# Optimization experiments

Measured on AMD Instinct MI355X. Metric: run time of the kernel, lower is better.

## Reference

```python
import jax, jax.numpy as jnp
import numpy as np

U, I, D, E = 8192, 8192, 64, 1048576  # users, items, emb dim, nnz of adjacency


def spmm(row, col, val, x, n):
    """Sparse (COO) @ dense: y[r] += val * x[c], like torch.sparse.mm."""
    return jax.ops.segment_sum(val[:, None] * x[col], row, num_segments=n)


def setup_inputs() -> dict:
    key = jax.random.key(0)
    k1, k2, k3, k4, k5, k6 = jax.random.split(key, 6)
    users_emb = jax.random.normal(k1, (U, D), dtype=jnp.float32) * 0.1  # nn.init.normal_(std=0.1)
    items_emb = jax.random.normal(k2, (I, D), dtype=jnp.float32) * 0.1
    edge_row = jax.random.randint(k3, (E,), 0, U + I, dtype=jnp.int32)
    edge_col = jax.random.randint(k4, (E,), 0, U + I, dtype=jnp.int32)
    # positive normalized adjacency values (stand-in for D^-1/2 A D^-1/2 entries)
    edge_val = jax.random.uniform(k5, (E,), dtype=jnp.float32) / 64.0
    # sparse 0/1 interaction matrix densified, as in labels = interaction_mat.toarray()
    labels = (jax.random.uniform(k6, (U, I)) < 0.02).astype(jnp.float32)
    return {"users_emb": users_emb, "items_emb": items_emb,
            "edge_row": edge_row, "edge_col": edge_col,
            "edge_val": edge_val, "labels": labels, "n_layers": 3}


def reference(users_emb, items_emb, edge_row, edge_col, edge_val, labels, n_layers):
    n = users_emb.shape[0] + items_emb.shape[0]
    u = users_emb.shape[0]
    all_emb = jnp.concatenate([users_emb, items_emb], axis=0)  # [n, D]
    # stack + mean over (n_layers+1) layer outputs == online accumulation
    acc = all_emb
    for _ in range(n_layers):
        all_emb = spmm(edge_row, edge_col, edge_val, all_emb, n)
        acc = acc + all_emb
    light_out = acc / jnp.float32(n_layers + 1)
    user_emb = light_out[:u]   # [U, D]
    item_emb = light_out[u:]   # [I, D]
    scores = user_emb @ item_emb.T  # [U, I]
    # BCEWithLogitsLoss (mean reduction): logaddexp(0, s) - s*y
    loss = jnp.mean(jnp.logaddexp(jnp.float32(0.0), scores) - scores * labels)
    return (loss, user_emb, item_emb)
```

## Files before the change

### kernel.cpp

```cpp
#include <hip/hip_runtime.h>

#define U_N 8192
#define I_N 8192
#define N_N 16384
#define D_N 64
#define E_N 1048576
#define CAP 128

typedef __attribute__((ext_vector_type(8)))  short short8;
typedef __attribute__((ext_vector_type(16))) float f32x16;


__global__ void k_prep(const float* __restrict__ ue, const float* __restrict__ ie,
                       float* __restrict__ cur, float* __restrict__ acc,
                       unsigned* __restrict__ cnt, float* __restrict__ lossp) {
    int i = blockIdx.x * blockDim.x + threadIdx.x;
    const int HU = U_N * D_N / 4;
    float4 v = (i < HU) ? ((const float4*)ue)[i] : ((const float4*)ie)[i - HU];
    ((float4*)cur)[i] = v;
    ((float4*)acc)[i] = v;
    if (i < N_N / 4) ((uint4*)cnt)[i] = make_uint4(0, 0, 0, 0);
    if (i == 0) *lossp = 0.f;
}

__global__ void k_bucket(const int* __restrict__ row, const int* __restrict__ col,
                         const float* __restrict__ val, unsigned* __restrict__ cnt,
                         int2* __restrict__ buckets) {
    int e = blockIdx.x * blockDim.x + threadIdx.x;
    if (e < E_N) {
        int r = row[e];
        unsigned p = atomicAdd(&cnt[r], 1u);
        if (p < CAP) buckets[(size_t)r * CAP + p] = make_int2(col[e], __float_as_int(val[e]));
    }
}

__global__ void k_spmm(const unsigned* __restrict__ cnt, const int4* __restrict__ bk4,
                       const float* __restrict__ x, float* __restrict__ y,
                       float* __restrict__ acc) {
    int wave = (int)((blockIdx.x * blockDim.x + threadIdx.x) >> 6);
    int lane = threadIdx.x & 63;
    if (wave >= N_N) return;
    int n = (int)cnt[wave]; n = n > CAP ? CAP : n;
    const int4* bp = bk4 + (size_t)wave * (CAP / 2);
    float a = 0.f;
    int j = 0;
    for (; j + 8 <= n; j += 8) {
        int4 q0 = bp[j / 2 + 0], q1 = bp[j / 2 + 1];
        int4 q2 = bp[j / 2 + 2], q3 = bp[j / 2 + 3];
        float x0 = x[q0.x * 64 + lane], x1 = x[q0.z * 64 + lane];
        float x2 = x[q1.x * 64 + lane], x3 = x[q1.z * 64 + lane];
        float x4 = x[q2.x * 64 + lane], x5 = x[q2.z * 64 + lane];
        float x6 = x[q3.x * 64 + lane], x7 = x[q3.z * 64 + lane];
        a = fmaf(__int_as_float(q0.y), x0, a); a = fmaf(__int_as_float(q0.w), x1, a);
        a = fmaf(__int_as_float(q1.y), x2, a); a = fmaf(__int_as_float(q1.w), x3, a);
        a = fmaf(__int_as_float(q2.y), x4, a); a = fmaf(__int_as_float(q2.w), x5, a);
        a = fmaf(__int_as_float(q3.y), x6, a); a = fmaf(__int_as_float(q3.w), x7, a);
    }
    const int2* bp2 = (const int2*)bp;
    for (; j < n; ++j) {
        int2 q = bp2[j];
        a = fmaf(__int_as_float(q.y), x[q.x * 64 + lane], a);
    }
    y[wave * 64 + lane] = a;
    acc[wave * 64 + lane] += a;
}

__global__ void k_spmm_last(const unsigned* __restrict__ cnt, const int4* __restrict__ bk4,
                            const float* __restrict__ x, const float* __restrict__ acc,
                            float* __restrict__ o, ushort* __restrict__ bfemb) {
    int wave = (int)((blockIdx.x * blockDim.x + threadIdx.x) >> 6);
    int lane = threadIdx.x & 63;
    if (wave >= N_N) return;
    int n = (int)cnt[wave]; n = n > CAP ? CAP : n;
    const int4* bp = bk4 + (size_t)wave * (CAP / 2);
    float a = 0.f;
    int j = 0;
    for (; j + 8 <= n; j += 8) {
        int4 q0 = bp[j / 2 + 0], q1 = bp[j / 2 + 1];
        int4 q2 = bp[j / 2 + 2], q3 = bp[j / 2 + 3];
        float x0 = x[q0.x * 64 + lane], x1 = x[q0.z * 64 + lane];
        float x2 = x[q1.x * 64 + lane], x3 = x[q1.z * 64 + lane];
        float x4 = x[q2.x * 64 + lane], x5 = x[q2.z * 64 + lane];
        float x6 = x[q3.x * 64 + lane], x7 = x[q3.z * 64 + lane];
        a = fmaf(__int_as_float(q0.y), x0, a); a = fmaf(__int_as_float(q0.w), x1, a);
        a = fmaf(__int_as_float(q1.y), x2, a); a = fmaf(__int_as_float(q1.w), x3, a);
        a = fmaf(__int_as_float(q2.y), x4, a); a = fmaf(__int_as_float(q2.w), x5, a);
        a = fmaf(__int_as_float(q3.y), x6, a); a = fmaf(__int_as_float(q3.w), x7, a);
    }
    const int2* bp2 = (const int2*)bp;
    for (; j < n; ++j) {
        int2 q = bp2[j];
        a = fmaf(__int_as_float(q.y), x[q.x * 64 + lane], a);
    }
    int idx = wave * 64 + lane;
    float l = (acc[idx] + a) * 0.25f;
    o[idx] = l;
    union { float f; unsigned u; } c; c.f = l;
    bfemb[idx] = (ushort)((c.u + 0x7fffu + ((c.u >> 16) & 1u)) >> 16);
}

__global__ __launch_bounds__(256) void k_gemm_loss(const ushort* __restrict__ bfemb,
                                                   const float* __restrict__ labels,
                                                   float* __restrict__ lossp) {
    __shared__ float red[4];
    int tid  = threadIdx.x;
    int lane = tid & 63;
    int w    = tid >> 6;
    int wr   = w >> 1, wc = w & 1;
    int row0 = blockIdx.y * 128 + wr * 64;
    int col0 = blockIdx.x * 128 + wc * 64;

    int lrow = lane & 31;
    int lk   = (lane >> 5) * 8;

    short8 a[2][4], b[2][4];
    #pragma unroll
    for (int fi = 0; fi < 2; ++fi) {
        const ushort* pa = bfemb + (size_t)(row0 + fi * 32 + lrow) * 64 + lk;
        const ushort* pb = bfemb + (size_t)(U_N + col0 + fi * 32 + lrow) * 64 + lk;
        #pragma unroll
        for (int kk = 0; kk < 4; ++kk) {
            a[fi][kk] = *(const short8*)(pa + kk * 16);
            b[fi][kk] = *(const short8*)(pb + kk * 16);
        }
    }

    f32x16 acc00 = {}, acc01 = {}, acc10 = {}, acc11 = {};
    #pragma unroll
    for (int kk = 0; kk < 4; ++kk) {
        acc00 = __builtin_amdgcn_mfma_f32_32x32x16_bf16(a[0][kk], b[0][kk], acc00, 0, 0, 0);
        acc01 = __builtin_amdgcn_mfma_f32_32x32x16_bf16(a[0][kk], b[1][kk], acc01, 0, 0, 0);
        acc10 = __builtin_amdgcn_mfma_f32_32x32x16_bf16(a[1][kk], b[0][kk], acc10, 0, 0, 0);
        acc11 = __builtin_amdgcn_mfma_f32_32x32x16_bf16(a[1][kk], b[1][kk], acc11, 0, 0, 0);
    }

    const float LN2 = 0.69314718055994531f;
    const float C2  = 0.125f;
    const float C4  = -1.0f / 192.0f;

    float sum = 0.f, maxa = 0.f;
    int rsub = (lane >> 5) * 4;
    #pragma unroll
    for (int fi = 0; fi < 2; ++fi) {
        #pragma unroll
        for (int fj = 0; fj < 2; ++fj) {
            const f32x16& ac = fi ? (fj ? acc11 : acc10) : (fj ? acc01 : acc00);
            int gcol = col0 + fj * 32 + (lane & 31);
            #pragma unroll
            for (int q = 0; q < 4; ++q) {
                #pragma unroll
                for (int r = 0; r < 4; ++r) {
                    int grow = row0 + fi * 32 + q * 8 + rsub + r;
                    float s = ac[q * 4 + r];
                    float lab = labels[(size_t)grow * 8192 + gcol];
                    float s2 = s * s;
                    float t = fmaf(s2, fmaf(s2, C4, C2), fmaf(s, 0.5f, LN2));
                    sum += t;
                    sum = fmaf(-s, lab, sum);
                    maxa = fmaxf(maxa, fabsf(s));
                }
            }
        }
    }

    if (__any(maxa > 1.0f)) {
        sum = 0.f;
        #pragma unroll
        for (int fi = 0; fi < 2; ++fi) {
            #pragma unroll
            for (int fj = 0; fj < 2; ++fj) {
                const f32x16& ac = fi ? (fj ? acc11 : acc10) : (fj ? acc01 : acc00);
                int gcol = col0 + fj * 32 + (lane & 31);
                #pragma unroll
                for (int q = 0; q < 4; ++q) {
                    #pragma unroll
                    for (int r = 0; r < 4; ++r) {
                        int grow = row0 + fi * 32 + q * 8 + rsub + r;
                        float s = ac[q * 4 + r];
                        float lab = labels[(size_t)grow * 8192 + gcol];
                        float t = fmaxf(s, 0.f) + __logf(1.f + __expf(-fabsf(s)));
                        sum += t - s * lab;
                    }
                }
            }
        }
    }

    #pragma unroll
    for (int off = 32; off > 0; off >>= 1) sum += __shfl_down(sum, off);
    if ((tid & 63) == 0) red[w] = sum;
    __syncthreads();
    if (tid == 0) atomicAdd(lossp, red[0] + red[1] + red[2] + red[3]);
}

__global__ void k_finish(const float* __restrict__ lossp, float* __restrict__ out) {
    out[0] = *lossp * (1.0f / 67108864.0f);
}

extern "C" void kernel_launch(void* const* d_in, const int* in_sizes, int n_in,
                              void* d_out, int out_size, void* d_ws, size_t ws_size,
                              hipStream_t stream) {
    const float* ue     = (const float*)d_in[0];
    const float* ie     = (const float*)d_in[1];
    const int*   erow   = (const int*)d_in[2];
    const int*   ecol   = (const int*)d_in[3];
    const float* eval_  = (const float*)d_in[4];
    const float* labels = (const float*)d_in[5];
    float* out = (float*)d_out;

    char* ws = (char*)d_ws;
    unsigned* cnt     = (unsigned*)(ws + 0);
    float*    lossp   = (float*)   (ws + 65536);
    int2*     buckets = (int2*)    (ws + 1048576);
    float*    emb0    = (float*)   (ws + 18874368);
    float*    emb1    = (float*)   (ws + 23068672);
    float*    accb    = (float*)   (ws + 27262976);
    ushort*   bfemb   = (ushort*)emb1;

    k_prep<<<1024, 256, 0, stream>>>(ue, ie, emb0, accb, cnt, lossp);
    k_bucket<<<4096, 256, 0, stream>>>(erow, ecol, eval_, cnt, buckets);

    const int4* bk4 = (const int4*)buckets;
    k_spmm<<<4096, 256, 0, stream>>>(cnt, bk4, emb0, emb1, accb);
    k_spmm<<<4096, 256, 0, stream>>>(cnt, bk4, emb1, emb0, accb);
    k_spmm_last<<<4096, 256, 0, stream>>>(cnt, bk4, emb0, accb, out + 1, bfemb);

    dim3 g(64, 64);
    k_gemm_loss<<<g, 256, 0, stream>>>(bfemb, labels, lossp);
    k_finish<<<1, 1, 0, stream>>>(lossp, out);
}
```

Before: 245.3 us.

## Store layer embeddings in bf16, pad bucket counters, fold finish into loss kernel

The intermediate layer embeddings read by the SpMM gathers are now stored as bf16, which halves gather traffic, while the layer accumulator stays in fp32. Bucket counters are spaced 16 words apart to reduce atomic contention from sharing the same cache line. The loss epilogue accumulates power sums of the scores and applies the series once per lane, and the separate finish kernel is replaced by a last-block-done counter. Rounding each layer's input to bf16 adds precision loss that compounds across layers.

```diff
diff --git a/kernel.cpp b/kernel.cpp
--- a/kernel.cpp
+++ b/kernel.cpp
@@ -1,26 +1,36 @@
 #include <hip/hip_runtime.h>
 
 #define U_N 8192
-#define I_N 8192
 #define N_N 16384
-#define D_N 64
 #define E_N 1048576
 #define CAP 128
+#define CSTRIDE 16
 
 typedef __attribute__((ext_vector_type(8)))  short short8;
 typedef __attribute__((ext_vector_type(16))) float f32x16;
 
 
+__device__ __forceinline__ float bfu(ushort u) {
+    union { unsigned v; float f; } c; c.v = (unsigned)u << 16; return c.f;
+}
+__device__ __forceinline__ ushort f2bf(float f) {
+    union { float f; unsigned u; } c; c.f = f;
+    return (ushort)((c.u + 0x7fffu + ((c.u >> 16) & 1u)) >> 16);
+}
+
 __global__ void k_prep(const float* __restrict__ ue, const float* __restrict__ ie,
-                       float* __restrict__ cur, float* __restrict__ acc,
-                       unsigned* __restrict__ cnt, float* __restrict__ lossp) {
+                       ushort* __restrict__ xb, float* __restrict__ acc,
+                       unsigned* __restrict__ cnt, float* __restrict__ lossp,
+                       unsigned* __restrict__ done) {
     int i = blockIdx.x * blockDim.x + threadIdx.x;
-    const int HU = U_N * D_N / 4;
+    const int HU = U_N * 64 / 4;
     float4 v = (i < HU) ? ((const float4*)ue)[i] : ((const float4*)ie)[i - HU];
-    ((float4*)cur)[i] = v;
     ((float4*)acc)[i] = v;
-    if (i < N_N / 4) ((uint4*)cnt)[i] = make_uint4(0, 0, 0, 0);
-    if (i == 0) *lossp = 0.f;
+    ushort4 b;
+    b.x = f2bf(v.x); b.y = f2bf(v.y); b.z = f2bf(v.z); b.w = f2bf(v.w);
+    ((ushort4*)xb)[i] = b;
+    if (i < 65536) ((uint4*)cnt)[i] = make_uint4(0, 0, 0, 0);
+    if (i == 0) { *lossp = 0.f; *done = 0u; }
 }
 
 __global__ void k_bucket(const int* __restrict__ row, const int* __restrict__ col,
@@ -29,28 +39,28 @@
     int e = blockIdx.x * blockDim.x + threadIdx.x;
     if (e < E_N) {
         int r = row[e];
-        unsigned p = atomicAdd(&cnt[r], 1u);
+        unsigned p = atomicAdd(&cnt[r * CSTRIDE], 1u);
         if (p < CAP) buckets[(size_t)r * CAP + p] = make_int2(col[e], __float_as_int(val[e]));
     }
 }
 
 __global__ void k_spmm(const unsigned* __restrict__ cnt, const int4* __restrict__ bk4,
-                       const float* __restrict__ x, float* __restrict__ y,
+                       const ushort* __restrict__ x, ushort* __restrict__ xo,
                        float* __restrict__ acc) {
     int wave = (int)((blockIdx.x * blockDim.x + threadIdx.x) >> 6);
     int lane = threadIdx.x & 63;
     if (wave >= N_N) return;
-    int n = (int)cnt[wave]; n = n > CAP ? CAP : n;
+    int n = (int)cnt[wave * CSTRIDE]; n = n > CAP ? CAP : n;
     const int4* bp = bk4 + (size_t)wave * (CAP / 2);
     float a = 0.f;
     int j = 0;
     for (; j + 8 <= n; j += 8) {
         int4 q0 = bp[j / 2 + 0], q1 = bp[j / 2 + 1];
         int4 q2 = bp[j / 2 + 2], q3 = bp[j / 2 + 3];
-        float x0 = x[q0.x * 64 + lane], x1 = x[q0.z * 64 + lane];
-        float x2 = x[q1.x * 64 + lane], x3 = x[q1.z * 64 + lane];
-        float x4 = x[q2.x * 64 + lane], x5 = x[q2.z * 64 + lane];
-        float x6 = x[q3.x * 64 + lane], x7 = x[q3.z * 64 + lane];
+        float x0 = bfu(x[q0.x * 64 + lane]), x1 = bfu(x[q0.z * 64 + lane]);
+        float x2 = bfu(x[q1.x * 64 + lane]), x3 = bfu(x[q1.z * 64 + lane]);
+        float x4 = bfu(x[q2.x * 64 + lane]), x5 = bfu(x[q2.z * 64 + lane]);
+        float x6 = bfu(x[q3.x * 64 + lane]), x7 = bfu(x[q3.z * 64 + lane]);
         a = fmaf(__int_as_float(q0.y), x0, a); a = fmaf(__int_as_float(q0.w), x1, a);
         a = fmaf(__int_as_float(q1.y), x2, a); a = fmaf(__int_as_float(q1.w), x3, a);
         a = fmaf(__int_as_float(q2.y), x4, a); a = fmaf(__int_as_float(q2.w), x5, a);
@@ -59,29 +69,30 @@
     const int2* bp2 = (const int2*)bp;
     for (; j < n; ++j) {
         int2 q = bp2[j];
-        a = fmaf(__int_as_float(q.y), x[q.x * 64 + lane], a);
-    }
-    y[wave * 64 + lane] = a;
-    acc[wave * 64 + lane] += a;
+        a = fmaf(__int_as_float(q.y), bfu(x[q.x * 64 + lane]), a);
+    }
+    int idx = wave * 64 + lane;
+    xo[idx] = f2bf(a);
+    acc[idx] += a;
 }
 
 __global__ void k_spmm_last(const unsigned* __restrict__ cnt, const int4* __restrict__ bk4,
-                            const float* __restrict__ x, const float* __restrict__ acc,
+                            const ushort* __restrict__ x, const float* __restrict__ acc,
                             float* __restrict__ o, ushort* __restrict__ bfemb) {
     int wave = (int)((blockIdx.x * blockDim.x + threadIdx.x) >> 6);
     int lane = threadIdx.x & 63;
     if (wave >= N_N) return;
-    int n = (int)cnt[wave]; n = n > CAP ? CAP : n;
+    int n = (int)cnt[wave * CSTRIDE]; n = n > CAP ? CAP : n;
     const int4* bp = bk4 + (size_t)wave * (CAP / 2);
     float a = 0.f;
     int j = 0;
     for (; j + 8 <= n; j += 8) {
         int4 q0 = bp[j / 2 + 0], q1 = bp[j / 2 + 1];
         int4 q2 = bp[j / 2 + 2], q3 = bp[j / 2 + 3];
-        float x0 = x[q0.x * 64 + lane], x1 = x[q0.z * 64 + lane];
-        float x2 = x[q1.x * 64 + lane], x3 = x[q1.z * 64 + lane];
-        float x4 = x[q2.x * 64 + lane], x5 = x[q2.z * 64 + lane];
-        float x6 = x[q3.x * 64 + lane], x7 = x[q3.z * 64 + lane];
+        float x0 = bfu(x[q0.x * 64 + lane]), x1 = bfu(x[q0.z * 64 + lane]);
+        float x2 = bfu(x[q1.x * 64 + lane]), x3 = bfu(x[q1.z * 64 + lane]);
+        float x4 = bfu(x[q2.x * 64 + lane]), x5 = bfu(x[q2.z * 64 + lane]);
+        float x6 = bfu(x[q3.x * 64 + lane]), x7 = bfu(x[q3.z * 64 + lane]);
         a = fmaf(__int_as_float(q0.y), x0, a); a = fmaf(__int_as_float(q0.w), x1, a);
         a = fmaf(__int_as_float(q1.y), x2, a); a = fmaf(__int_as_float(q1.w), x3, a);
         a = fmaf(__int_as_float(q2.y), x4, a); a = fmaf(__int_as_float(q2.w), x5, a);
@@ -90,18 +101,19 @@
     const int2* bp2 = (const int2*)bp;
     for (; j < n; ++j) {
         int2 q = bp2[j];
-        a = fmaf(__int_as_float(q.y), x[q.x * 64 + lane], a);
+        a = fmaf(__int_as_float(q.y), bfu(x[q.x * 64 + lane]), a);
     }
     int idx = wave * 64 + lane;
     float l = (acc[idx] + a) * 0.25f;
     o[idx] = l;
-    union { float f; unsigned u; } c; c.f = l;
-    bfemb[idx] = (ushort)((c.u + 0x7fffu + ((c.u >> 16) & 1u)) >> 16);
+    bfemb[idx] = f2bf(l);
 }
 
 __global__ __launch_bounds__(256) void k_gemm_loss(const ushort* __restrict__ bfemb,
                                                    const float* __restrict__ labels,
-                                                   float* __restrict__ lossp) {
+                                                   float* __restrict__ lossp,
+                                                   unsigned* __restrict__ done,
+                                                   float* __restrict__ out) {
     __shared__ float red[4];
     int tid  = threadIdx.x;
     int lane = tid & 63;
@@ -134,11 +146,7 @@
         acc11 = __builtin_amdgcn_mfma_f32_32x32x16_bf16(a[1][kk], b[1][kk], acc11, 0, 0, 0);
     }
 
-    const float LN2 = 0.69314718055994531f;
-    const float C2  = 0.125f;
-    const float C4  = -1.0f / 192.0f;
-
-    float sum = 0.f, maxa = 0.f;
+    float sum1 = 0.f, sum2 = 0.f, sum4 = 0.f, sumL = 0.f, m2 = 0.f;
     int rsub = (lane >> 5) * 4;
     #pragma unroll
     for (int fi = 0; fi < 2; ++fi) {
@@ -154,47 +162,50 @@
                     float s = ac[q * 4 + r];
                     float lab = labels[(size_t)grow * 8192 + gcol];
                     float s2 = s * s;
-                    float t = fmaf(s2, fmaf(s2, C4, C2), fmaf(s, 0.5f, LN2));
-                    sum += t;
-                    sum = fmaf(-s, lab, sum);
-                    maxa = fmaxf(maxa, fabsf(s));
+                    sum1 += s;
+                    sum2 += s2;
+                    sum4 = fmaf(s2, s2, sum4);
+                    sumL = fmaf(s, lab, sumL);
+                    m2 = fmaxf(m2, s2);
                 }
             }
         }
     }
 
-    if (__any(maxa > 1.0f)) {
-        sum = 0.f;
+    const float LN2 = 0.69314718055994531f;
+    float base = fmaf(0.5f, sum1, fmaf(0.125f, sum2, fmaf(-1.f / 192.f, sum4, 64.f * LN2)));
+
+    if (__any(m2 > 1.0f)) {
+        base = 0.f;
         #pragma unroll
         for (int fi = 0; fi < 2; ++fi) {
             #pragma unroll
             for (int fj = 0; fj < 2; ++fj) {
                 const f32x16& ac = fi ? (fj ? acc11 : acc10) : (fj ? acc01 : acc00);
-                int gcol = col0 + fj * 32 + (lane & 31);
                 #pragma unroll
-                for (int q = 0; q < 4; ++q) {
-                    #pragma unroll
-                    for (int r = 0; r < 4; ++r) {
-                        int grow = row0 + fi * 32 + q * 8 + rsub + r;
-                        float s = ac[q * 4 + r];
-                        float lab = labels[(size_t)grow * 8192 + gcol];
-                        float t = fmaxf(s, 0.f) + __logf(1.f + __expf(-fabsf(s)));
-                        sum += t - s * lab;
-                    }
+                for (int t = 0; t < 16; ++t) {
+                    float s = ac[t];
+                    base += fmaxf(s, 0.f) + __logf(1.f + __expf(-fabsf(s)));
                 }
             }
         }
     }
 
+    float sum = base - sumL;
     #pragma unroll
     for (int off = 32; off > 0; off >>= 1) sum += __shfl_down(sum, off);
     if ((tid & 63) == 0) red[w] = sum;
     __syncthreads();
-    if (tid == 0) atomicAdd(lossp, red[0] + red[1] + red[2] + red[3]);
-}
-
-__global__ void k_finish(const float* __restrict__ lossp, float* __restrict__ out) {
-    out[0] = *lossp * (1.0f / 67108864.0f);
+    if (tid == 0) {
+        atomicAdd(lossp, red[0] + red[1] + red[2] + red[3]);
+        __threadfence();
+        unsigned t = atomicAdd(done, 1u);
+        if (t == 64u * 64u - 1u) {
+            __threadfence();
+            float total = atomicAdd(lossp, 0.0f);
+            out[0] = total * (1.0f / 67108864.0f);
+        }
+    }
 }
 
 extern "C" void kernel_launch(void* const* d_in, const int* in_sizes, int n_in,
@@ -210,22 +221,22 @@
 
     char* ws = (char*)d_ws;
     unsigned* cnt     = (unsigned*)(ws + 0);
-    float*    lossp   = (float*)   (ws + 65536);
-    int2*     buckets = (int2*)    (ws + 1048576);
-    float*    emb0    = (float*)   (ws + 18874368);
-    float*    emb1    = (float*)   (ws + 23068672);
-    float*    accb    = (float*)   (ws + 27262976);
-    ushort*   bfemb   = (ushort*)emb1;
-
-    k_prep<<<1024, 256, 0, stream>>>(ue, ie, emb0, accb, cnt, lossp);
+    float*    lossp   = (float*)   (ws + 1048576);
+    unsigned* done    = (unsigned*)(ws + 1048580);
+    ushort*   xb0     = (ushort*)  (ws + 1048832);
+    ushort*   xb1     = (ushort*)  (ws + 3145984);
+    float*    accb    = (float*)   (ws + 5243136);
+    ushort*   bfemb   = (ushort*)  (ws + 9437440);
+    int2*     buckets = (int2*)    (ws + 11534592);
+
+    k_prep<<<1024, 256, 0, stream>>>(ue, ie, xb0, accb, cnt, lossp, done);
     k_bucket<<<4096, 256, 0, stream>>>(erow, ecol, eval_, cnt, buckets);
 
     const int4* bk4 = (const int4*)buckets;
-    k_spmm<<<4096, 256, 0, stream>>>(cnt, bk4, emb0, emb1, accb);
-    k_spmm<<<4096, 256, 0, stream>>>(cnt, bk4, emb1, emb0, accb);
-    k_spmm_last<<<4096, 256, 0, stream>>>(cnt, bk4, emb0, accb, out + 1, bfemb);
+    k_spmm<<<4096, 256, 0, stream>>>(cnt, bk4, xb0, xb1, accb);
+    k_spmm<<<4096, 256, 0, stream>>>(cnt, bk4, xb1, xb0, accb);
+    k_spmm_last<<<4096, 256, 0, stream>>>(cnt, bk4, xb0, accb, out + 1, bfemb);
 
     dim3 g(64, 64);
-    k_gemm_loss<<<g, 256, 0, stream>>>(bfemb, labels, lossp);
-    k_finish<<<1, 1, 0, stream>>>(lossp, out);
-}
+    k_gemm_loss<<<g, 256, 0, stream>>>(bfemb, labels, lossp, done, out);
+}
```

Measured after the change: 315.2 us. +28.5%, slower.
